# Kernel tuning notes

Measured on AMD Instinct MI355X. Metric: run time of the kernel, lower is better.

The kernel has to match this reference:

```python
import jax, jax.numpy as jnp
import numpy as np

N_HEAD = 8
NORM_GROUPS = 32
EPS = 1e-6


def setup_inputs() -> dict:
    key = jax.random.key(0)
    ks = jax.random.split(key, 9)
    B, C, H, W, D = 1, 256, 16, 16, 16
    COND = 512
    x = jax.random.normal(ks[0], (B, C, H, W, D), dtype=jnp.float32)
    cond = jax.random.normal(ks[1], (B, COND), dtype=jnp.float32)
    # AdaGN linear scale/shift (torch Linear: weight [C, cond_dim], bias [C])
    w_scale = jax.random.normal(ks[2], (C, COND), dtype=jnp.float32) * 0.02
    b_scale = jax.random.normal(ks[3], (C,), dtype=jnp.float32) * 0.02
    w_shift = jax.random.normal(ks[4], (C, COND), dtype=jnp.float32) * 0.02
    b_shift = jax.random.normal(ks[5], (C,), dtype=jnp.float32) * 0.02
    # 1x1x1 conv3d weights collapse to matrices: qkv [3C, C] (no bias), out [C, C] + bias
    w_qkv = jax.random.normal(ks[6], (3 * C, C), dtype=jnp.float32) * (1.0 / np.sqrt(C))
    w_out = jax.random.normal(ks[7], (C, C), dtype=jnp.float32) * (1.0 / np.sqrt(C))
    b_out = jax.random.normal(ks[8], (C,), dtype=jnp.float32) * 0.02
    return {"x": x, "cond": cond, "w_scale": w_scale, "b_scale": b_scale,
            "w_shift": w_shift, "b_shift": b_shift, "w_qkv": w_qkv,
            "w_out": w_out, "b_out": b_out}


def _ada_gn(x, cond, w_scale, b_scale, w_shift, b_shift):
    B, C, H, W, D = x.shape
    G = NORM_GROUPS
    xg = x.reshape(B, G, C // G, H, W, D)
    mean = jnp.mean(xg, axis=(2, 3, 4, 5), keepdims=True)
    var = jnp.var(xg, axis=(2, 3, 4, 5), keepdims=True)
    x_norm = ((xg - mean) * jax.lax.rsqrt(var + EPS)).reshape(B, C, H, W, D)
    scale = (cond @ w_scale.T + b_scale)[:, :, None, None, None]  # [B,C,1,1,1]
    shift = (cond @ w_shift.T + b_shift)[:, :, None, None, None]
    return x_norm * (1.0 + scale) + shift


def reference(x, cond, w_scale, b_scale, w_shift, b_shift, w_qkv, w_out, b_out):
    B, C, H, W, D = x.shape
    nh = N_HEAD
    hd = C // nh
    N = H * W * D  # flattened spatial tokens
    norm = _ada_gn(x, cond, w_scale, b_scale, w_shift, b_shift)
    # 1x1x1 conv == channel matmul
    qkv = jnp.einsum('oc,bchwd->bohwd', w_qkv, norm)        # [B,3C,H,W,D]
    qkv = qkv.reshape(B, nh, 3 * hd, N)
    q, k, v = jnp.split(qkv, 3, axis=2)                      # each [B,nh,hd,N]
    attn = jnp.einsum('bnci,bncj->bnij', q, k) / jnp.sqrt(jnp.float32(C))
    attn = jax.nn.softmax(attn, axis=-1)                     # [B,nh,N,N]
    out = jnp.einsum('bnij,bncj->bnci', attn, v)             # [B,nh,hd,N]
    out = out.reshape(B, C, H, W, D)
    out = jnp.einsum('oc,bchwd->bohwd', w_out, out) + b_out[None, :, None, None, None]
    return out + x
```

## Files before the change

kernel.cpp:

```cpp
#include <hip/hip_runtime.h>
#include <math.h>

#define CCH 256
#define NN  4096
#define NHEAD 8
#define CONDD 512

typedef __attribute__((ext_vector_type(8))) short short8;
typedef __attribute__((ext_vector_type(4))) float f32x4;
typedef __attribute__((ext_vector_type(16))) float f32x16;

static __device__ __forceinline__ short f2bf(float f) {
    union { float f; uint32_t u; } v; v.f = f;
    uint32_t r = v.u + 0x7fffu + ((v.u >> 16) & 1u);
    return (short)(r >> 16);
}

static __device__ __forceinline__ uint32_t cvt_pk_bf16(float a, float b) {
    uint32_t r;
    asm("v_cvt_pk_bf16_f32 %0, %1, %2" : "=v"(r) : "v"(a), "v"(b));
    return r;
}

__global__ __launch_bounds__(256) void front_fused(const float* __restrict__ x,
                                                   const float* __restrict__ cond,
                                                   const float* __restrict__ w_scale,
                                                   const float* __restrict__ b_scale,
                                                   const float* __restrict__ w_shift,
                                                   const float* __restrict__ b_shift,
                                                   const float* __restrict__ wq,
                                                   const float* __restrict__ wo,
                                                   float* __restrict__ partial,
                                                   float* __restrict__ scale,
                                                   float* __restrict__ shift,
                                                   short* __restrict__ wqb,
                                                   short* __restrict__ wob) {
    __shared__ float rs[4], rss[4];
    int bb = blockIdx.x;
    int t = threadIdx.x;
    if (bb < 256) {
        const float4* p = (const float4*)(x + bb * 4096);
        float s = 0.f, ss = 0.f;
        for (int k = t; k < 1024; k += 256) {
            float4 v = p[k];
            s += v.x + v.y + v.z + v.w;
            ss += v.x * v.x + v.y * v.y + v.z * v.z + v.w * v.w;
        }
        #pragma unroll
        for (int off = 32; off; off >>= 1) { s += __shfl_xor(s, off); ss += __shfl_xor(ss, off); }
        int wid = t >> 6;
        if ((t & 63) == 0) { rs[wid] = s; rss[wid] = ss; }
        __syncthreads();
        if (t == 0) {
            partial[2 * bb] = rs[0] + rs[1] + rs[2] + rs[3];
            partial[2 * bb + 1] = rss[0] + rss[1] + rss[2] + rss[3];
        }
    } else if (bb < 1280) {
        int idx = (bb - 256) * 256 + t;
        if (idx < 196608) wqb[idx] = f2bf(wq[idx]);
        else              wob[idx - 196608] = f2bf(wo[idx - 196608]);
    } else {
        int o = (bb - 1280) * 4 + (t >> 6);
        int lane = t & 63;
        float ds = 0.f, dh = 0.f;
        for (int k = lane; k < CONDD; k += 64) {
            float cv = cond[k];
            ds += cv * w_scale[o * CONDD + k];
            dh += cv * w_shift[o * CONDD + k];
        }
        #pragma unroll
        for (int off = 32; off; off >>= 1) { ds += __shfl_xor(ds, off); dh += __shfl_xor(dh, off); }
        if (lane == 0) { scale[o] = ds + b_scale[o]; shift[o] = dh + b_shift[o]; }
    }
}

__global__ __launch_bounds__(256) void normalize_t(const float* __restrict__ x,
                                                   const float* __restrict__ partial,
                                                   const float* __restrict__ scale,
                                                   const float* __restrict__ shift,
                                                   short* __restrict__ norm_t) {
    __shared__ float gm[8], gr[8];
    __shared__ float Aa[64], Bb[64];
    __shared__ short tile[32 * 66];
    int i0 = blockIdx.x * 32;
    int c0 = blockIdx.y * 64;
    int g0 = c0 >> 3;
    int t = threadIdx.x;
    if (t < 8) {
        float s = 0.f, ss = 0.f;
        #pragma unroll
        for (int ch = 0; ch < 8; ++ch) {
            s += partial[((g0 + t) * 8 + ch) * 2];
            ss += partial[((g0 + t) * 8 + ch) * 2 + 1];
        }
        float mean = s * (1.0f / 32768.0f);
        float var = ss * (1.0f / 32768.0f) - mean * mean;
        gm[t] = mean;
        gr[t] = rsqrtf(var + 1e-6f);
    }
    __syncthreads();
    if (t < 64) {
        int c = c0 + t;
        float a = gr[t >> 3] * (1.0f + scale[c]);
        Aa[t] = a;
        Bb[t] = shift[c] - gm[t >> 3] * a;
    }
    __syncthreads();
    #pragma unroll
    for (int e0 = 0; e0 < 8; ++e0) {
        int e = e0 * 256 + t;
        int cl = e >> 5, il = e & 31;
        float v = x[(c0 + cl) * NN + i0 + il];
        tile[il * 66 + cl] = f2bf(v * Aa[cl] + Bb[cl]);
    }
    __syncthreads();
    #pragma unroll
    for (int e0 = 0; e0 < 4; ++e0) {
        int e = e0 * 256 + t;
        int il = e >> 5, cd = e & 31;
        uint32_t d = *(const uint32_t*)&tile[il * 66 + 2 * cd];
        *(uint32_t*)&norm_t[(i0 + il) * 256 + c0 + 2 * cd] = d;
    }
}

__global__ __launch_bounds__(256) void qkv_gemm(const short* __restrict__ wqb,
                                                const short* __restrict__ norm_t,
                                                short* __restrict__ qtb, short* __restrict__ ktb,
                                                short* __restrict__ vcb) {
    int t = threadIdx.x;
    int w = t >> 6, lane = t & 63, li = lane & 15, lg = lane >> 4;
    int o0 = blockIdx.x * 32;
    int i0 = blockIdx.y * 64 + w * 16;
    f32x4 acc[2] = {{0,0,0,0},{0,0,0,0}};
    const short* bbase = norm_t + (i0 + li) * 256 + 8 * lg;
    const short* abase = wqb + (o0 + li) * 256 + 8 * lg;
    #pragma unroll
    for (int ks = 0; ks < 8; ++ks) {
        short8 bfrag = *(const short8*)(bbase + ks * 32);
        #pragma unroll
        for (int f = 0; f < 2; ++f) {
            short8 afrag = *(const short8*)(abase + f * 16 * 256 + ks * 32);
            acc[f] = __builtin_amdgcn_mfma_f32_16x16x32_bf16(afrag, bfrag, acc[f], 0, 0, 0);
        }
    }
    int i = i0 + li;
    #pragma unroll
    for (int f = 0; f < 2; ++f) {
        #pragma unroll
        for (int r = 0; r < 4; ++r) {
            int o = o0 + 16 * f + 4 * lg + r;
            float v = acc[f][r];
            int h = o / 96;
            int rr = o - h * 96;
            int cc = rr & 31;
            int kind = rr >> 5;
            if (kind == 0)      qtb[(h * NN + i) * 32 + cc] = f2bf(v * (0.0625f * 1.44269504f));
            else if (kind == 1) ktb[(h * NN + i) * 32 + cc] = f2bf(v);
            else                vcb[(h * 32 + cc) * NN + i] = f2bf(v);
        }
    }
}

__global__ __launch_bounds__(512, 6) void attention_mfma(const short* __restrict__ qtb,
                                                         const short* __restrict__ ktb,
                                                         const short* __restrict__ vcb,
                                                         short* __restrict__ attnT) {
    __shared__ float lds_acc[8][32][32];
    __shared__ float lds_lsum[8][32];

    int bid = blockIdx.x;
    int h = bid & 7;
    int i_base = (bid >> 3) * 32;
    int t = threadIdx.x;
    int w = t >> 6, lane = t & 63, l31 = lane & 31, hi = lane >> 5;

    const short* qrow = qtb + (h * NN + i_base + l31) * 32;
    short8 qf0 = *(const short8*)(qrow + 8 * hi);
    short8 qf1 = *(const short8*)(qrow + 16 + 8 * hi);

    const short* kp = ktb + (h * NN + w * 512 + l31) * 32 + 8 * hi;
    const short* vp = vcb + (h * 32 + l31) * NN + w * 512 + 8 * hi;

    f32x16 acc = {0,0,0,0,0,0,0,0,0,0,0,0,0,0,0,0};
    const f32x16 zero16 = {0,0,0,0,0,0,0,0,0,0,0,0,0,0,0,0};
    float lsum = 0.f;

    #pragma unroll 1
    for (int tile = 0; tile < 16; ++tile) {
        short8 k0 = *(const short8*)kp;
        short8 k1 = *(const short8*)(kp + 16);
        short8 v0 = *(const short8*)vp;
        short8 v1 = *(const short8*)(vp + 16);
        kp += 1024;
        vp += 32;

        __builtin_amdgcn_s_setprio(1);
        f32x16 s = __builtin_amdgcn_mfma_f32_32x32x16_bf16(k0, qf0, zero16, 0, 0, 0);
        s = __builtin_amdgcn_mfma_f32_32x32x16_bf16(k1, qf1, s, 0, 0, 0);
        __builtin_amdgcn_s_setprio(0);

        float p[16];
        #pragma unroll
        for (int r = 0; r < 16; ++r) p[r] = __builtin_amdgcn_exp2f(s[r]);

        float u0 = 0.f, u1 = 0.f;
        #pragma unroll
        for (int r = 0; r < 4; ++r) { u0 += p[r] + p[4 + r]; u1 += p[8 + r] + p[12 + r]; }
        lsum += u0 + u1;

        auto A1 = __builtin_amdgcn_permlane32_swap(cvt_pk_bf16(p[0], p[1]),   cvt_pk_bf16(p[4], p[5]),   false, false);
        auto A2 = __builtin_amdgcn_permlane32_swap(cvt_pk_bf16(p[2], p[3]),   cvt_pk_bf16(p[6], p[7]),   false, false);
        auto A3 = __builtin_amdgcn_permlane32_swap(cvt_pk_bf16(p[8], p[9]),   cvt_pk_bf16(p[12], p[13]), false, false);
        auto A4 = __builtin_amdgcn_permlane32_swap(cvt_pk_bf16(p[10], p[11]), cvt_pk_bf16(p[14], p[15]), false, false);

        union PF { uint32_t u[4]; short8 s8; };
        PF f1, f2;
        f1.u[0] = A1[0]; f1.u[1] = A2[0]; f1.u[2] = A1[1]; f1.u[3] = A2[1];
        f2.u[0] = A3[0]; f2.u[1] = A4[0]; f2.u[2] = A3[1]; f2.u[3] = A4[1];

        __builtin_amdgcn_s_setprio(1);
        acc = __builtin_amdgcn_mfma_f32_32x32x16_bf16(v0, f1.s8, acc, 0, 0, 0);
        acc = __builtin_amdgcn_mfma_f32_32x32x16_bf16(v1, f2.s8, acc, 0, 0, 0);
        __builtin_amdgcn_s_setprio(0);
    }

    lsum += __shfl_xor(lsum, 32);

    #pragma unroll
    for (int r = 0; r < 16; ++r) {
        int c = (r & 3) + 8 * (r >> 2) + 4 * hi;
        lds_acc[w][c][l31] = acc[r];
    }
    if (hi == 0) lds_lsum[w][l31] = lsum;
    __syncthreads();

    if (t < 256) {
        int q = t & 31, c0 = (t >> 5) * 4;
        float s0 = 0.f, s1 = 0.f, s2 = 0.f, s3 = 0.f, ls = 0.f;
        #pragma unroll
        for (int ww = 0; ww < 8; ++ww) {
            s0 += lds_acc[ww][c0 + 0][q];
            s1 += lds_acc[ww][c0 + 1][q];
            s2 += lds_acc[ww][c0 + 2][q];
            s3 += lds_acc[ww][c0 + 3][q];
            ls += lds_lsum[ww][q];
        }
        float inv = 1.0f / ls;
        uint2 uu;
        uu.x = cvt_pk_bf16(s0 * inv, s1 * inv);
        uu.y = cvt_pk_bf16(s2 * inv, s3 * inv);
        *(uint2*)&attnT[(i_base + q) * 256 + h * 32 + c0] = uu;
    }
}

__global__ __launch_bounds__(256) void proj_gemm(const short* __restrict__ wob,
                                                 const short* __restrict__ attnT,
                                                 const float* __restrict__ b_out,
                                                 const float* __restrict__ x,
                                                 float* __restrict__ out) {
    int t = threadIdx.x;
    int w = t >> 6, lane = t & 63, li = lane & 15, lg = lane >> 4;
    int o0 = blockIdx.x * 32;
    int i0 = blockIdx.y * 64 + w * 16;
    f32x4 acc[2] = {{0,0,0,0},{0,0,0,0}};
    const short* bbase = attnT + (i0 + li) * 256 + 8 * lg;
    const short* abase = wob + (o0 + li) * 256 + 8 * lg;
    #pragma unroll
    for (int ks = 0; ks < 8; ++ks) {
        short8 bfrag = *(const short8*)(bbase + ks * 32);
        #pragma unroll
        for (int f = 0; f < 2; ++f) {
            short8 afrag = *(const short8*)(abase + f * 16 * 256 + ks * 32);
            acc[f] = __builtin_amdgcn_mfma_f32_16x16x32_bf16(afrag, bfrag, acc[f], 0, 0, 0);
        }
    }
    int i = i0 + li;
    #pragma unroll
    for (int f = 0; f < 2; ++f) {
        #pragma unroll
        for (int r = 0; r < 4; ++r) {
            int o = o0 + 16 * f + 4 * lg + r;
            out[o * NN + i] = acc[f][r] + b_out[o] + x[o * NN + i];
        }
    }
}

extern "C" void kernel_launch(void* const* d_in, const int* in_sizes, int n_in,
                              void* d_out, int out_size, void* d_ws, size_t ws_size,
                              hipStream_t stream) {
    const float* x       = (const float*)d_in[0];
    const float* cond    = (const float*)d_in[1];
    const float* w_scale = (const float*)d_in[2];
    const float* b_scale = (const float*)d_in[3];
    const float* w_shift = (const float*)d_in[4];
    const float* b_shift = (const float*)d_in[5];
    const float* w_qkv   = (const float*)d_in[6];
    const float* w_out   = (const float*)d_in[7];
    const float* b_out   = (const float*)d_in[8];
    float* out = (float*)d_out;

    float* ws = (float*)d_ws;
    float* scale   = ws;
    float* shift   = ws + 256;
    float* partial = ws + 512;
    short* norm_t = (short*)(ws + 1024);
    short* qtb = norm_t + 1048576;
    short* ktb = qtb + 1048576;
    short* vcb = ktb + 1048576;
    short* attnT = vcb + 1048576;
    short* wqb = attnT + 1048576;
    short* wob = wqb + 768 * 256;

    front_fused<<<1344, 256, 0, stream>>>(x, cond, w_scale, b_scale, w_shift, b_shift,
                                          w_qkv, w_out, partial, scale, shift, wqb, wob);
    normalize_t<<<dim3(128, 4), 256, 0, stream>>>(x, partial, scale, shift, norm_t);
    qkv_gemm<<<dim3(24, 64), 256, 0, stream>>>(wqb, norm_t, qtb, ktb, vcb);
    attention_mfma<<<1024, 512, 0, stream>>>(qtb, ktb, vcb, attnT);
    proj_gemm<<<dim3(8, 64), 256, 0, stream>>>(wob, attnT, b_out, x, out);
}
```

Baseline: 87.32 us.

## Stage K/V tiles in LDS with async double buffering and split-K attention merge

The attention kernel now processes 128 queries per block, split across 4 waves, and covers half of the keys per block (split-K in two). K and V tiles are staged into swizzled LDS buffers with global_load_lds, double-buffered so they are shared by all waves rather than each wave loading its own key range. Partial accumulators and row sums go to global memory, and a new merge kernel sums the two halves, normalizes, and writes bf16 attnT. This trades per-wave redundant global loads and the in-block cross-wave reduction for an extra kernel launch, extra global traffic for the fp32 partials, and a barrier per tile.

```diff
diff --git a/kernel.cpp b/kernel.cpp
--- a/kernel.cpp
+++ b/kernel.cpp
@@ -161,96 +161,136 @@
     }
 }
 
-__global__ __launch_bounds__(512, 6) void attention_mfma(const short* __restrict__ qtb,
+__global__ __launch_bounds__(256, 4) void attention_mfma(const short* __restrict__ qtb,
                                                          const short* __restrict__ ktb,
                                                          const short* __restrict__ vcb,
-                                                         short* __restrict__ attnT) {
-    __shared__ float lds_acc[8][32][32];
-    __shared__ float lds_lsum[8][32];
+                                                         float* __restrict__ pacc,
+                                                         float* __restrict__ plsum) {
+    __shared__ __align__(16) short kbuf[2][2048];
+    __shared__ __align__(16) short vbuf[2][2048];
 
     int bid = blockIdx.x;
     int h = bid & 7;
-    int i_base = (bid >> 3) * 32;
+    int qb = (bid >> 3) & 31;
+    int kh = bid >> 8;
     int t = threadIdx.x;
     int w = t >> 6, lane = t & 63, l31 = lane & 31, hi = lane >> 5;
 
-    const short* qrow = qtb + (h * NN + i_base + l31) * 32;
+    int qbase = qb * 128 + w * 32;
+    const short* qrow = qtb + (h * NN + qbase + l31) * 32;
     short8 qf0 = *(const short8*)(qrow + 8 * hi);
     short8 qf1 = *(const short8*)(qrow + 16 + 8 * hi);
 
-    const short* kp = ktb + (h * NN + w * 512 + l31) * 32 + 8 * hi;
-    const short* vp = vcb + (h * 32 + l31) * NN + w * 512 + 8 * hi;
+    int kr_ = t >> 2, ks_ = t & 3, kg_ = ks_ ^ (kr_ & 3);
+    int vr_ = t >> 3, vs_ = t & 7, vg_ = vs_ ^ (vr_ & 7);
+    const char* kgbase = (const char*)(ktb + (h * NN + kh * 2048) * 32) + kr_ * 64 + kg_ * 16;
+    const char* vgbase = (const char*)(vcb + (h * 32 + vr_) * NN + kh * 2048) + vg_ * 16;
+    int wave_off = (t >> 6) * 1024;
 
     f32x16 acc = {0,0,0,0,0,0,0,0,0,0,0,0,0,0,0,0};
     const f32x16 zero16 = {0,0,0,0,0,0,0,0,0,0,0,0,0,0,0,0};
     float lsum = 0.f;
 
+    __builtin_amdgcn_global_load_lds((const uint32_t*)kgbase, (uint32_t*)((char*)&kbuf[0][0] + wave_off), 16, 0, 0);
+    __builtin_amdgcn_global_load_lds((const uint32_t*)vgbase, (uint32_t*)((char*)&vbuf[0][0] + wave_off), 16, 0, 0);
+    __syncthreads();
+
     #pragma unroll 1
-    for (int tile = 0; tile < 16; ++tile) {
-        short8 k0 = *(const short8*)kp;
-        short8 k1 = *(const short8*)(kp + 16);
-        short8 v0 = *(const short8*)vp;
-        short8 v1 = *(const short8*)(vp + 16);
-        kp += 1024;
-        vp += 32;
-
-        __builtin_amdgcn_s_setprio(1);
-        f32x16 s = __builtin_amdgcn_mfma_f32_32x32x16_bf16(k0, qf0, zero16, 0, 0, 0);
-        s = __builtin_amdgcn_mfma_f32_32x32x16_bf16(k1, qf1, s, 0, 0, 0);
-        __builtin_amdgcn_s_setprio(0);
-
-        float p[16];
-        #pragma unroll
-        for (int r = 0; r < 16; ++r) p[r] = __builtin_amdgcn_exp2f(s[r]);
-
-        float u0 = 0.f, u1 = 0.f;
-        #pragma unroll
-        for (int r = 0; r < 4; ++r) { u0 += p[r] + p[4 + r]; u1 += p[8 + r] + p[12 + r]; }
-        lsum += u0 + u1;
-
-        auto A1 = __builtin_amdgcn_permlane32_swap(cvt_pk_bf16(p[0], p[1]),   cvt_pk_bf16(p[4], p[5]),   false, false);
-        auto A2 = __builtin_amdgcn_permlane32_swap(cvt_pk_bf16(p[2], p[3]),   cvt_pk_bf16(p[6], p[7]),   false, false);
-        auto A3 = __builtin_amdgcn_permlane32_swap(cvt_pk_bf16(p[8], p[9]),   cvt_pk_bf16(p[12], p[13]), false, false);
-        auto A4 = __builtin_amdgcn_permlane32_swap(cvt_pk_bf16(p[10], p[11]), cvt_pk_bf16(p[14], p[15]), false, false);
-
-        union PF { uint32_t u[4]; short8 s8; };
-        PF f1, f2;
-        f1.u[0] = A1[0]; f1.u[1] = A2[0]; f1.u[2] = A1[1]; f1.u[3] = A2[1];
-        f2.u[0] = A3[0]; f2.u[1] = A4[0]; f2.u[2] = A3[1]; f2.u[3] = A4[1];
-
-        __builtin_amdgcn_s_setprio(1);
-        acc = __builtin_amdgcn_mfma_f32_32x32x16_bf16(v0, f1.s8, acc, 0, 0, 0);
-        acc = __builtin_amdgcn_mfma_f32_32x32x16_bf16(v1, f2.s8, acc, 0, 0, 0);
-        __builtin_amdgcn_s_setprio(0);
+    for (int st = 0; st < 32; ++st) {
+        int cur = st & 1;
+        if (st < 31) {
+            const char* kn = kgbase + (st + 1) * 4096;
+            const char* vn = vgbase + (st + 1) * 128;
+            __builtin_amdgcn_global_load_lds((const uint32_t*)kn, (uint32_t*)((char*)&kbuf[cur ^ 1][0] + wave_off), 16, 0, 0);
+            __builtin_amdgcn_global_load_lds((const uint32_t*)vn, (uint32_t*)((char*)&vbuf[cur ^ 1][0] + wave_off), 16, 0, 0);
+        }
+
+        #pragma unroll
+        for (int half = 0; half < 2; ++half) {
+            int jl = half * 32;
+            int R = jl + l31;
+            const short* kr = &kbuf[cur][R * 32];
+            int rx = R & 3;
+            short8 kf0 = *(const short8*)(kr + ((hi ^ rx) << 3));
+            short8 kf1 = *(const short8*)(kr + (((2 + hi) ^ rx) << 3));
+            const short* vr = &vbuf[cur][l31 * 64];
+            int cx = l31 & 7;
+            int s0 = (jl >> 3) + hi;
+            short8 vf0 = *(const short8*)(vr + ((s0 ^ cx) << 3));
+            short8 vf1 = *(const short8*)(vr + (((s0 + 2) ^ cx) << 3));
+
+            __builtin_amdgcn_s_setprio(1);
+            f32x16 s = __builtin_amdgcn_mfma_f32_32x32x16_bf16(kf0, qf0, zero16, 0, 0, 0);
+            s = __builtin_amdgcn_mfma_f32_32x32x16_bf16(kf1, qf1, s, 0, 0, 0);
+            __builtin_amdgcn_s_setprio(0);
+
+            float p[16];
+            #pragma unroll
+            for (int r = 0; r < 16; ++r) p[r] = __builtin_amdgcn_exp2f(s[r]);
+
+            float u0 = 0.f, u1 = 0.f;
+            #pragma unroll
+            for (int r = 0; r < 4; ++r) { u0 += p[r] + p[4 + r]; u1 += p[8 + r] + p[12 + r]; }
+            lsum += u0 + u1;
+
+            auto A1 = __builtin_amdgcn_permlane32_swap(cvt_pk_bf16(p[0], p[1]),   cvt_pk_bf16(p[4], p[5]),   false, false);
+            auto A2 = __builtin_amdgcn_permlane32_swap(cvt_pk_bf16(p[2], p[3]),   cvt_pk_bf16(p[6], p[7]),   false, false);
+            auto A3 = __builtin_amdgcn_permlane32_swap(cvt_pk_bf16(p[8], p[9]),   cvt_pk_bf16(p[12], p[13]), false, false);
+            auto A4 = __builtin_amdgcn_permlane32_swap(cvt_pk_bf16(p[10], p[11]), cvt_pk_bf16(p[14], p[15]), false, false);
+
+            union PF { uint32_t u[4]; short8 s8; };
+            PF f1, f2;
+            f1.u[0] = A1[0]; f1.u[1] = A2[0]; f1.u[2] = A1[1]; f1.u[3] = A2[1];
+            f2.u[0] = A3[0]; f2.u[1] = A4[0]; f2.u[2] = A3[1]; f2.u[3] = A4[1];
+
+            __builtin_amdgcn_s_setprio(1);
+            acc = __builtin_amdgcn_mfma_f32_32x32x16_bf16(vf0, f1.s8, acc, 0, 0, 0);
+            acc = __builtin_amdgcn_mfma_f32_32x32x16_bf16(vf1, f2.s8, acc, 0, 0, 0);
+            __builtin_amdgcn_s_setprio(0);
+        }
+        __syncthreads();
     }
 
     lsum += __shfl_xor(lsum, 32);
 
+    int qg = qbase + l31;
+    float* pb = pacc + ((kh * 8 + h) * 32) * NN + qg;
     #pragma unroll
     for (int r = 0; r < 16; ++r) {
         int c = (r & 3) + 8 * (r >> 2) + 4 * hi;
-        lds_acc[w][c][l31] = acc[r];
-    }
-    if (hi == 0) lds_lsum[w][l31] = lsum;
-    __syncthreads();
-
-    if (t < 256) {
-        int q = t & 31, c0 = (t >> 5) * 4;
-        float s0 = 0.f, s1 = 0.f, s2 = 0.f, s3 = 0.f, ls = 0.f;
-        #pragma unroll
-        for (int ww = 0; ww < 8; ++ww) {
-            s0 += lds_acc[ww][c0 + 0][q];
-            s1 += lds_acc[ww][c0 + 1][q];
-            s2 += lds_acc[ww][c0 + 2][q];
-            s3 += lds_acc[ww][c0 + 3][q];
-            ls += lds_lsum[ww][q];
-        }
-        float inv = 1.0f / ls;
-        uint2 uu;
-        uu.x = cvt_pk_bf16(s0 * inv, s1 * inv);
-        uu.y = cvt_pk_bf16(s2 * inv, s3 * inv);
-        *(uint2*)&attnT[(i_base + q) * 256 + h * 32 + c0] = uu;
-    }
+        pb[c * NN] = acc[r];
+    }
+    if (hi == 0) plsum[(kh * 8 + h) * NN + qg] = lsum;
+}
+
+__global__ __launch_bounds__(256) void attn_merge(const float* __restrict__ pacc,
+                                                  const float* __restrict__ plsum,
+                                                  short* __restrict__ attnT) {
+    __shared__ float tile[64][33];
+    __shared__ float invl[64];
+    int it = blockIdx.x;
+    int h = blockIdx.y;
+    int t = threadIdx.x;
+    int i0 = it * 64;
+    int c = t >> 3, ic = (t & 7) * 8;
+    const float* p0 = pacc + (h * 32 + c) * NN + i0 + ic;
+    const float* p1 = pacc + ((8 + h) * 32 + c) * NN + i0 + ic;
+    #pragma unroll
+    for (int k = 0; k < 8; ++k) tile[ic + k][c] = p0[k] + p1[k];
+    if (t < 64) {
+        float ls = plsum[h * NN + i0 + t] + plsum[(8 + h) * NN + i0 + t];
+        invl[t] = 1.0f / ls;
+    }
+    __syncthreads();
+    int i = t >> 2, cs = (t & 3) * 8;
+    float iv = invl[i];
+    const float* tr = &tile[i][cs];
+    uint4 o;
+    o.x = cvt_pk_bf16(tr[0] * iv, tr[1] * iv);
+    o.y = cvt_pk_bf16(tr[2] * iv, tr[3] * iv);
+    o.z = cvt_pk_bf16(tr[4] * iv, tr[5] * iv);
+    o.w = cvt_pk_bf16(tr[6] * iv, tr[7] * iv);
+    *(uint4*)&attnT[(i0 + i) * 256 + h * 32 + cs] = o;
 }
 
 __global__ __launch_bounds__(256) void proj_gemm(const short* __restrict__ wob,
@@ -310,11 +350,14 @@
     short* attnT = vcb + 1048576;
     short* wqb = attnT + 1048576;
     short* wob = wqb + 768 * 256;
+    float* pacc  = (float*)(wob + 65536);
+    float* plsum = pacc + 2 * 8 * 32 * NN;
 
     front_fused<<<1344, 256, 0, stream>>>(x, cond, w_scale, b_scale, w_shift, b_shift,
                                           w_qkv, w_out, partial, scale, shift, wqb, wob);
     normalize_t<<<dim3(128, 4), 256, 0, stream>>>(x, partial, scale, shift, norm_t);
     qkv_gemm<<<dim3(24, 64), 256, 0, stream>>>(wqb, norm_t, qtb, ktb, vcb);
-    attention_mfma<<<1024, 512, 0, stream>>>(qtb, ktb, vcb, attnT);
+    attention_mfma<<<512, 256, 0, stream>>>(qtb, ktb, vcb, pacc, plsum);
+    attn_merge<<<dim3(64, 8), 256, 0, stream>>>(pacc, plsum, attnT);
     proj_gemm<<<dim3(8, 64), 256, 0, stream>>>(wob, attnT, b_out, x, out);
 }
```

Result: faster. 76.64 us (median of 2 runs) (-12.2%).
